# Kernel tuning notes

Hardware: AMD Instinct MI355X
Metric: run time of the kernel (lower is better)

Reference implementation:

```python
import jax, jax.numpy as jnp
import numpy as np

B, L, P = 65536, 512, 96
E_LIN, E = 14, 16
FFT = 512
TEMP = 0.07
K = 2
EPS = 1e-5


def setup_inputs() -> dict:
    key = jax.random.key(0)
    k0, k1, k2 = jax.random.split(key, 3)
    x = jax.random.normal(k0, (B, L), dtype=jnp.float32)
    Wg = jax.random.normal(k1, (E, FFT // 2), dtype=jnp.float32) * 0.02
    bg = jnp.zeros((E,), dtype=jnp.float32)
    Wr = jax.random.normal(k2, (E_LIN, P, L), dtype=jnp.float32) * 0.02
    br = jnp.zeros((E_LIN, P), dtype=jnp.float32)
    return {"x": x, "Wg": Wg, "bg": bg, "Wr": Wr, "br": br}


def _periodogram(x):
    # x: [B, L] -> normalized power spectrum [B, FFT//2]
    x0 = x - jnp.mean(x, axis=1, keepdims=True)
    dft = jnp.fft.fft(x0, n=FFT, axis=1) / np.float32(np.sqrt(FFT))
    dft = dft[:, : FFT // 2]
    I = dft.real ** 2 + dft.imag ** 2
    s = jnp.sum(I, axis=1, keepdims=True)
    s = jnp.where(s == 0, jnp.ones_like(s), s)
    return I / s


def reference(x, Wg, bg, Wr, br):
    # gating (eval mode: no noise, divide by temperature)
    I = _periodogram(x)                                  # [B, F/2]
    gate = (I @ Wg.T + bg) / TEMP                        # [B, E]
    topv, topi = jax.lax.top_k(gate, K)                  # [B, K]
    gates = jax.nn.softmax(topv, axis=1)                 # [B, K]

    # RLinear experts: RevIN(norm) -> Linear -> RevIN(denorm); stats detached
    mu = jax.lax.stop_gradient(jnp.mean(x, axis=1, keepdims=True))        # [B,1]
    sd = jax.lax.stop_gradient(jnp.sqrt(jnp.var(x, axis=1, keepdims=True) + EPS))
    xn = (x - mu) / sd                                   # [B, L]
    yr = jnp.einsum('bl,epl->bep', xn, Wr) + br          # [B, E_LIN, P]
    yr = yr * sd[:, :, None] + mu[:, :, None]

    mean_out = jnp.broadcast_to(jnp.mean(x, axis=1, keepdims=True), (x.shape[0], P))[:, None, :]
    naive_out = jnp.broadcast_to(x[:, -1:], (x.shape[0], P))[:, None, :]

    eo = jnp.concatenate([yr, mean_out, naive_out], axis=1)   # [B, E, P]
    sel = jnp.take_along_axis(eo, topi[:, :, None], axis=1)   # [B, K, P]
    out = jnp.sum(gates[:, :, None] * sel, axis=1)            # [B, P]
    return out
```

## Files before the change

### kernel.cpp

```cpp
#include <hip/hip_runtime.h>
#include <math.h>

#define NB_B 65536
#define NL   512
#define NP   96
#define NE   16
#define NEL  14
#define NF   256
#define TEMP_INV (1.0f/0.07f)
#define TAU  1e-5f
#define PI_D 3.14159265358979323846
#define MAXCHK 1280

typedef __attribute__((ext_vector_type(8))) short bf16x8;
typedef __attribute__((ext_vector_type(4))) float f32x4;


#define WS_PCNT     0
#define WS_PTK      16384
#define WS_PBASE    32768
#define WS_FLAGCNT  33792
#define WS_NCHK     33824
#define WS_FLAG     33856
#define WS_SSUM     296000
#define WS_WGT      301376
#define WS_BGT      317760
#define WS_TWF      317824
#define WS_TWD      319872
#define WS_REC      328064
#define WS_HDR      590208
#define WS_RIDX     1638784
#define WS_WRB      1900928
#define WS_DESC     3473792

__device__ __forceinline__ unsigned short f2bf(float f) {
    unsigned u = __float_as_uint(f);
    unsigned r = (u + 0x7fffu + ((u >> 16) & 1u)) >> 16;
    return (unsigned short)r;
}

__global__ __launch_bounds__(256) void k_prep(
    const float* __restrict__ Wg, const float* __restrict__ bg,
    const float* __restrict__ Wr,
    float* __restrict__ Ssum, float* __restrict__ WgE, float* __restrict__ bgT,
    float2* __restrict__ twf, double2* __restrict__ twd,
    int* __restrict__ pcnt, int* __restrict__ flagcnt,
    ushort4* __restrict__ Wrb)
{
    int g = blockIdx.x * 256 + threadIdx.x;
    {
        ushort4 o = make_ushort4(0, 0, 0, 0);
        if (g < NEL * NP * NL / 4) {
            float4 v = ((const float4*)Wr)[g];
            o.x = f2bf(v.x); o.y = f2bf(v.y); o.z = f2bf(v.z); o.w = f2bf(v.w);
        }
        Wrb[g] = o;
    }
    if (g < NEL * NP) {
        const float4* w = (const float4*)(Wr + (size_t)g * NL);
        float s = 0.f;
        for (int i = 0; i < NL / 4; i++) { float4 v = w[i]; s += v.x + v.y + v.z + v.w; }
        Ssum[g] = s;
    }
    if (g < 4096) {
        int c = g & 3, e = (g >> 2) & 15, f4 = g >> 6;
        WgE[g] = Wg[e * NF + f4 * 4 + c] * TEMP_INV;
    }
    if (g < NF) {
        double a = -2.0 * PI_D * (double)g / 512.0;
        twf[g] = make_float2((float)cos(a), (float)sin(a));
    }
    if (g < 512) {
        double a = -2.0 * PI_D * (double)g / 512.0;
        twd[g] = make_double2(cos(a), sin(a));
    }
    if (g < 256) pcnt[g << 4] = 0;
    if (g < NE) bgT[g] = bg[g] * TEMP_INV;
    if (g == 300) *flagcnt = 0;
}

__global__ __launch_bounds__(256) void k_gate(
    const float* __restrict__ x,
    const float4* __restrict__ WgE4, const float* __restrict__ bgT,
    const float2* __restrict__ twf,
    int* __restrict__ rec, float4* __restrict__ hdr,
    int* __restrict__ flaglist, int* __restrict__ flagcnt,
    int* __restrict__ pcnt)
{
    __shared__ float2 s_tw[256];
    __shared__ __align__(16) float2 s_z[4][576];
    float* s_Iv = (float*)&s_z[0][0];

    const int t = threadIdx.x;
    const int wv = t >> 6, l = t & 63;
    const int b0 = blockIdx.x * 8 + wv * 2;
    s_tw[t] = twf[t];

    const float* xa = x + (size_t)b0 * NL;
    const float* xb = xa + NL;
    float xr[8], xi[8];
#pragma unroll
    for (int k = 0; k < 8; k++) { xr[k] = xa[k * 64 + l]; xi[k] = xb[k * 64 + l]; }
    const float last_a = __shfl(xr[7], 63);
    const float last_b = __shfl(xi[7], 63);
    __syncthreads();

#pragma unroll
    for (int k = 0; k < 4; k++) {
        float2 w = s_tw[k * 64 + l];
        float ur = xr[k], ui = xi[k], vr = xr[k + 4], vi = xi[k + 4];
        xr[k] = ur + vr; xi[k] = ui + vi;
        float dr = ur - vr, di = ui - vi;
        xr[k + 4] = dr * w.x - di * w.y; xi[k + 4] = dr * w.y + di * w.x;
    }
    {
        const int kk[4] = {0, 1, 4, 5};
#pragma unroll
        for (int g2 = 0; g2 < 4; g2++) {
            int k = kk[g2];
            float2 w = s_tw[((k & 1) * 64 + l) << 1];
            float ur = xr[k], ui = xi[k], vr = xr[k + 2], vi = xi[k + 2];
            xr[k] = ur + vr; xi[k] = ui + vi;
            float dr = ur - vr, di = ui - vi;
            xr[k + 2] = dr * w.x - di * w.y; xi[k + 2] = dr * w.y + di * w.x;
        }
    }
    {
        float2 w = s_tw[l << 2];
#pragma unroll
        for (int k = 0; k < 8; k += 2) {
            float ur = xr[k], ui = xi[k], vr = xr[k + 1], vi = xi[k + 1];
            xr[k] = ur + vr; xi[k] = ui + vi;
            float dr = ur - vr, di = ui - vi;
            xr[k + 1] = dr * w.x - di * w.y; xi[k + 1] = dr * w.y + di * w.x;
        }
    }
#pragma unroll
    for (int st = 3; st < 9; st++) {
        const int half = 256 >> st;
        const int tt = (l & (half - 1)) << st;
        float2 w = s_tw[tt];
        const bool up = (l & half) != 0;
        const float sg = up ? -1.f : 1.f;
        const float cc = up ? w.x : 1.f;
        const float ss = up ? w.y : 0.f;
#pragma unroll
        for (int k = 0; k < 8; k++) {
            float pr = __shfl_xor(xr[k], half);
            float pi = __shfl_xor(xi[k], half);
            float tr = fmaf(sg, xr[k], pr);
            float ti = fmaf(sg, xi[k], pi);
            xr[k] = tr * cc - ti * ss;
            xi[k] = tr * ss + ti * cc;
        }
    }

#pragma unroll
    for (int k = 0; k < 8; k++) {
        int i = k * 64 + l;
        s_z[wv][i + (i >> 3)] = make_float2(xr[k], xi[k]);
    }

    float Ia[4], Ib[4];
    float psa = 0.f, psb = 0.f;
#pragma unroll
    for (int j = 0; j < 4; j++) {
        int f = (l << 2) | j;
        int i1_ = (int)(__brev((unsigned)f) >> 23);
        int i2_ = (int)(__brev((unsigned)((512 - f) & 511)) >> 23);
        float2 z1 = s_z[wv][i1_ + (i1_ >> 3)];
        float2 z2 = s_z[wv][i2_ + (i2_ >> 3)];
        float pr_ = z1.x + z2.x, qm = z1.y - z2.y;
        float qp = z1.y + z2.y, pm = z1.x - z2.x;
        float va = pr_ * pr_ + qm * qm;
        float vb = qp * qp + pm * pm;
        if (f == 0) { va = 0.f; vb = 0.f; }
        Ia[j] = va; Ib[j] = vb;
        psa += va; psb += vb;
    }
#pragma unroll
    for (int m = 1; m < 64; m <<= 1) {
        psa += __shfl_xor(psa, m); psb += __shfl_xor(psb, m);
    }
    const float psa_raw = psa, psb_raw = psb;
    if (psa == 0.f) psa = 1.f;
    if (psb == 0.f) psb = 1.f;
    const float inv_a = 1.f / psa, inv_b = 1.f / psb;

    const float2 Z0   = s_z[wv][0];
    const float2 Z256 = s_z[wv][1];

    float* wI = s_Iv + wv * 1152;
    const int io = (l << 2) + ((l >> 4) << 2);
    *(float4*)(wI + io)       = make_float4(Ia[0], Ia[1], Ia[2], Ia[3]);
    *(float4*)(wI + 272 + io) = make_float4(Ib[0], Ib[1], Ib[2], Ib[3]);

    const int e16 = l & 15, cq = l >> 4;
    const float bgv = bgT[e16];
    float accA = 0.f, accB = 0.f;
    const float* rA = wI + cq * 68;
    const float* rB = rA + 272;
#pragma unroll 4
    for (int jj = 0; jj < 16; jj++) {
        float4 ia = *(const float4*)(rA + 4 * jj);
        float4 ib = *(const float4*)(rB + 4 * jj);
        float4 w = WgE4[(cq * 16 + jj) * 16 + e16];
        accA += ia.x * w.x + ia.y * w.y + ia.z * w.z + ia.w * w.w;
        accB += ib.x * w.x + ib.y * w.y + ib.z * w.z + ib.w * w.w;
    }
    accA += __shfl_xor(accA, 16); accA += __shfl_xor(accA, 32);
    accB += __shfl_xor(accB, 16); accB += __shfl_xor(accB, 32);

    float v = ((l & 16) ? accB * inv_b : accA * inv_a) + bgv;

    float b0v = v; int b0i = e16;
#pragma unroll
    for (int m = 1; m < 16; m <<= 1) {
        float ov = __shfl_xor(b0v, m); int oi = __shfl_xor(b0i, m);
        if (ov > b0v || (ov == b0v && oi < b0i)) { b0v = ov; b0i = oi; }
    }
    float v1 = (e16 == b0i) ? -1e30f : v;
    float b1v = v1; int b1i = e16;
#pragma unroll
    for (int m = 1; m < 16; m <<= 1) {
        float ov = __shfl_xor(b1v, m); int oi = __shfl_xor(b1i, m);
        if (ov > b1v || (ov == b1v && oi < b1i)) { b1v = ov; b1i = oi; }
    }
    float v2 = (e16 == b1i) ? -1e30f : v1;
    float b2v = v2;
#pragma unroll
    for (int m = 1; m < 16; m <<= 1) {
        float ov = __shfl_xor(b2v, m);
        b2v = fmaxf(b2v, ov);
    }

    if (l == 0 || l == 16) {
        const int r = l >> 4;
        const int b = b0 + r;
        const float mu = (r ? Z0.y : Z0.x) * (1.f / 512.f);
        const float Jv = r ? Z256.y : Z256.x;
        const float ps = r ? psb_raw : psa_raw;
        const float sd = sqrtf((0.5f * ps + Jv * Jv) * (1.f / 262144.f) + 1e-5f);
        const float last = r ? last_b : last_a;
        const float w0 = 1.f / (1.f + expf(b1v - b0v));
        const int pid = b0i * 16 + b1i;
        rec[b] = pid;
        hdr[b] = make_float4(mu, sd, last, w0);
        atomicAdd(&pcnt[pid << 4], 1);
        if (b1v - b2v < TAU) {
            int pos = atomicAdd(flagcnt, 1);
            flaglist[pos] = b;
        }
    }
}

__global__ __launch_bounds__(256) void k_refine(
    const float* __restrict__ x, const double2* __restrict__ twd,
    const float* __restrict__ Wg, const float* __restrict__ bg,
    int* __restrict__ rec, float4* __restrict__ hdr,
    const int* __restrict__ flaglist, const int* __restrict__ flagcnt,
    int* __restrict__ pcnt)
{
    __shared__ double s_x[512];
    __shared__ double s_I[256];
    __shared__ double s_red[16];
    __shared__ double s_g[16];
    const int nf = *flagcnt;
    const int t = threadIdx.x;
    const int wid = t >> 6, lane = t & 63;
    for (int fi = blockIdx.x; fi < nf; fi += gridDim.x) {
        const int b = flaglist[fi];
        const float* xp = x + (size_t)b * NL;
        double v0 = (double)xp[t], v1 = (double)xp[t + 256];
        double lsum = v0 + v1;
        for (int m = 1; m < 64; m <<= 1) lsum += __shfl_xor(lsum, m);
        if (lane == 0) s_red[wid] = lsum;
        __syncthreads();
        double mu = (s_red[0] + s_red[1] + s_red[2] + s_red[3]) * (1.0 / 512.0);
        s_x[t] = v0 - mu; s_x[t + 256] = v1 - mu;
        __syncthreads();
        double2 w = twd[t];
        double pr = 1.0, pi = 0.0, cr = 0.0, ci = 0.0;
        for (int n = 0; n < 512; n++) {
            double xv = s_x[n];
            cr += xv * pr; ci += xv * pi;
            double t2 = pr * w.x - pi * w.y;
            pi = pr * w.y + pi * w.x;
            pr = t2;
        }
        double I = cr * cr + ci * ci;
        s_I[t] = I;
        double ls = I;
        for (int m = 1; m < 64; m <<= 1) ls += __shfl_xor(ls, m);
        if (lane == 0) s_red[8 + wid] = ls;
        __syncthreads();
        double stot = s_red[8] + s_red[9] + s_red[10] + s_red[11];
        if (stot == 0.0) stot = 1.0;
        if (t < 16) {
            double acc = 0.0;
            const float* wrow = Wg + t * NF;
            for (int f = 0; f < NF; f++) acc += s_I[f] * (double)wrow[f];
            s_g[t] = (acc / stot + (double)bg[t]) * (1.0 / 0.07);
        }
        __syncthreads();
        if (t == 0) {
            double c0 = -1e300, c1 = -1e300; int j0 = 0, j1 = 0;
            for (int i = 0; i < 16; i++) {
                double v = s_g[i];
                if (v > c0) { c1 = c0; j1 = j0; c0 = v; j0 = i; }
                else if (v > c1) { c1 = v; j1 = i; }
            }
            double e1 = exp(c1 - c0);
            float w0f = (float)(1.0 / (1.0 + e1));
            int newpid = j0 * 16 + j1;
            int old = rec[b];
            if (newpid != old) {
                atomicSub(&pcnt[old << 4], 1);
                atomicAdd(&pcnt[newpid << 4], 1);
                rec[b] = newpid;
            }
            ((float*)(hdr + b))[3] = w0f;
        }
        __syncthreads();
    }
}

__global__ __launch_bounds__(256) void k_scan(
    const int* __restrict__ pcnt, int* __restrict__ pbase, int* __restrict__ ptk,
    int* __restrict__ desc, int* __restrict__ nchk)
{
    __shared__ int s[256], c[256];
    const int t = threadIdx.x;
    const int n = pcnt[t << 4];
    s[t] = n;
    c[t] = (n + 63) >> 6;
    __syncthreads();
    for (int off = 1; off < 256; off <<= 1) {
        int v1 = (t >= off) ? s[t - off] : 0;
        int v2 = (t >= off) ? c[t - off] : 0;
        __syncthreads();
        s[t] += v1; c[t] += v2;
        __syncthreads();
    }
    int excl = t ? s[t - 1] : 0;
    int cexcl = t ? c[t - 1] : 0;
    pbase[t] = excl;
    ptk[t << 4] = excl;
    int myc = (n + 63) >> 6;
    for (int j = 0; j < myc; j++) desc[cexcl + j] = (t << 16) | j;
    if (t == 255) *nchk = cexcl + myc;
}

__global__ __launch_bounds__(256) void k_scatter(
    const int* __restrict__ rec, int* __restrict__ ptk, int* __restrict__ ridx)
{
    __shared__ int h[256], base_[256];
    const int t = threadIdx.x;
    const int b = blockIdx.x * 256 + t;
    h[t] = 0;
    __syncthreads();
    int pid = rec[b];
    int lo = atomicAdd(&h[pid], 1);
    __syncthreads();
    if (h[t]) base_[t] = atomicAdd(&ptk[t << 4], h[t]);
    __syncthreads();
    ridx[base_[pid] + lo] = b;
}

__global__ __launch_bounds__(256) void k_gemm(
    const float* __restrict__ x, const unsigned short* __restrict__ Wrb,
    const float* __restrict__ br, const float* __restrict__ Ssum,
    const float4* __restrict__ hdr, float* __restrict__ out,
    const int* __restrict__ pcnt, const int* __restrict__ pbase,
    const int* __restrict__ ridx,
    const int* __restrict__ desc, const int* __restrict__ nchk)
{
    __shared__ __align__(16) unsigned short sA[64 * 72];
    __shared__ __align__(16) unsigned short sB[2][96 * 72];
    __shared__ int    s_idx[64];
    __shared__ float4 s_hdr[64];
    __shared__ float  s_br[2][96], s_S[2][96];
    if ((int)blockIdx.x >= *nchk) return;
    const int d = desc[blockIdx.x];
    const int pid = d >> 16, cc = d & 0xffff;
    const int n = pcnt[pid << 4];
    const int base = pbase[pid];
    const int i0 = pid >> 4, i1 = pid & 15;
    const int t = threadIdx.x;
    const int lane = t & 63, wv = t >> 6;
    const int quad = lane >> 4, l16 = lane & 15;
    const int ar = t >> 2, asub = t & 3;
    if (t < 96) {
        s_br[0][t] = (i0 < NEL) ? br[i0 * NP + t] : 0.f;
        s_S [0][t] = (i0 < NEL) ? Ssum[i0 * NP + t] : 0.f;
        s_br[1][t] = (i1 < NEL) ? br[i1 * NP + t] : 0.f;
        s_S [1][t] = (i1 < NEL) ? Ssum[i1 * NP + t] : 0.f;
    }
    if (t < 64) {
        int g = cc * 64 + t;
        bool vld = g < n;
        int row = vld ? ridx[base + g] : -1;
        s_idx[t] = row;
        s_hdr[t] = vld ? hdr[row] : make_float4(0.f, 0.f, 0.f, 0.f);
    }
    const unsigned short* wb0 = Wrb + (size_t)i0 * NP * NL;
    const unsigned short* wb1 = Wrb + (size_t)i1 * NP * NL;
    __syncthreads();

    f32x4 acc[2][6];
#pragma unroll
    for (int ex = 0; ex < 2; ex++)
#pragma unroll
        for (int j = 0; j < 6; j++) acc[ex][j] = (f32x4){0.f, 0.f, 0.f, 0.f};
    int rr = s_idx[ar]; if (rr < 0) rr = s_idx[0];
    const float* xrow = x + (size_t)rr * NL + asub * 16;

    for (int kb = 0; kb < NL; kb += 64) {
        {
            const float4* src = (const float4*)(xrow + kb);
            unsigned short tmp[16];
#pragma unroll
            for (int i = 0; i < 4; i++) {
                float4 v = src[i];
                tmp[i * 4 + 0] = f2bf(v.x); tmp[i * 4 + 1] = f2bf(v.y);
                tmp[i * 4 + 2] = f2bf(v.z); tmp[i * 4 + 3] = f2bf(v.w);
            }
            unsigned short* dst = sA + ar * 72 + asub * 16;
            *(bf16x8*)dst       = *(bf16x8*)tmp;
            *(bf16x8*)(dst + 8) = *(bf16x8*)(tmp + 8);
        }
#pragma unroll
        for (int it = 0; it < 6; it++) {
            int ex = (it >= 3);
            int fl = t + (it - 3 * ex) * 256;
            int p = fl >> 3, kg = fl & 7;
            const unsigned short* wb = ex ? wb1 : wb0;
            bf16x8 v = *(const bf16x8*)(wb + (size_t)p * NL + kb + kg * 8);
            *(bf16x8*)(&sB[ex][p * 72 + kg * 8]) = v;
        }
        __syncthreads();
#pragma unroll
        for (int ks = 0; ks < 2; ks++) {
            bf16x8 af = *(const bf16x8*)(sA + (wv * 16 + l16) * 72 + ks * 32 + quad * 8);
#pragma unroll
            for (int ex = 0; ex < 2; ex++)
#pragma unroll
                for (int nt = 0; nt < 6; nt++) {
                    bf16x8 bf = *(const bf16x8*)(&sB[ex][(nt * 16 + l16) * 72 + ks * 32 + quad * 8]);
                    acc[ex][nt] = __builtin_amdgcn_mfma_f32_16x16x32_bf16(af, bf, acc[ex][nt], 0, 0, 0);
                }
        }
        __syncthreads();
    }
#pragma unroll
    for (int i = 0; i < 4; i++) {
        int rloc = wv * 16 + quad * 4 + i;
        int row = s_idx[rloc];
        if (row >= 0) {
            float4 h = s_hdr[rloc];
            float mu = h.x, sd = h.y, last = h.z, w0 = h.w, w1 = 1.f - w0;
            float* orow = out + (size_t)row * NP;
#pragma unroll
            for (int nt = 0; nt < 6; nt++) {
                int p = nt * 16 + l16;
                float v0 = (i0 < NEL) ? (mu + s_br[0][p] * sd - mu * s_S[0][p] + acc[0][nt][i])
                                      : (i0 == NEL ? mu : last);
                float v1 = (i1 < NEL) ? (mu + s_br[1][p] * sd - mu * s_S[1][p] + acc[1][nt][i])
                                      : (i1 == NEL ? mu : last);
                orow[p] = w0 * v0 + w1 * v1;
            }
        }
    }
}

extern "C" void kernel_launch(void* const* d_in, const int* in_sizes, int n_in,
                              void* d_out, int out_size, void* d_ws, size_t ws_size,
                              hipStream_t stream)
{
    const float* x  = (const float*)d_in[0];
    const float* Wg = (const float*)d_in[1];
    const float* bg = (const float*)d_in[2];
    const float* Wr = (const float*)d_in[3];
    const float* br = (const float*)d_in[4];
    float* out = (float*)d_out;
    char* ws = (char*)d_ws;

    int*     pcnt     = (int*)(ws + WS_PCNT);
    int*     ptk      = (int*)(ws + WS_PTK);
    int*     pbase    = (int*)(ws + WS_PBASE);
    int*     flagcnt  = (int*)(ws + WS_FLAGCNT);
    int*     nchk     = (int*)(ws + WS_NCHK);
    int*     flaglist = (int*)(ws + WS_FLAG);
    float*   Ssum     = (float*)(ws + WS_SSUM);
    float*   WgE      = (float*)(ws + WS_WGT);
    float*   bgT      = (float*)(ws + WS_BGT);
    float2*  twf      = (float2*)(ws + WS_TWF);
    double2* twd      = (double2*)(ws + WS_TWD);
    int*     rec      = (int*)(ws + WS_REC);
    float4*  hdr      = (float4*)(ws + WS_HDR);
    int*     ridx     = (int*)(ws + WS_RIDX);
    unsigned short* Wrb = (unsigned short*)(ws + WS_WRB);
    int*     desc     = (int*)(ws + WS_DESC);

    k_prep<<<dim3(768), dim3(256), 0, stream>>>(Wg, bg, Wr, Ssum, WgE, bgT, twf, twd,
                                                pcnt, flagcnt, (ushort4*)Wrb);
    k_gate<<<dim3(NB_B / 8), dim3(256), 0, stream>>>(x, (const float4*)WgE, bgT, twf,
                                                     rec, hdr, flaglist, flagcnt, pcnt);
    k_refine<<<dim3(512), dim3(256), 0, stream>>>(x, twd, Wg, bg, rec, hdr,
                                                  flaglist, flagcnt, pcnt);
    k_scan<<<dim3(1), dim3(256), 0, stream>>>(pcnt, pbase, ptk, desc, nchk);
    k_scatter<<<dim3(NB_B / 256), dim3(256), 0, stream>>>(rec, ptk, ridx);
    k_gemm<<<dim3(MAXCHK), dim3(256), 0, stream>>>(x, Wrb, br, Ssum, hdr, out,
                                                   pcnt, pbase, ridx, desc, nchk);
}
```

Measured before the change: 320.7 us.

## Cache bf16 copy of x in gate kernel and register-prefetch GEMM tiles

The gate kernel now writes a bf16 copy of x to workspace when space allows, so the GEMM reads half the bytes and skips the per-tile conversion. The GEMM prefetches the next A and B tiles into registers while the current tile is computed. FFT twiddles are held in registers instead of shared memory, and the last butterfly stage drops its trivial multiply. The cost is an extra bf16 write pass over x in the gate kernel, and the fast path depends on the workspace being large enough.

```diff
diff --git a/kernel.cpp b/kernel.cpp
--- a/kernel.cpp
+++ b/kernel.cpp
@@ -32,6 +32,7 @@
 #define WS_RIDX     1638784
 #define WS_WRB      1900928
 #define WS_DESC     3473792
+#define WS_XB16     3480064
 
 __device__ __forceinline__ unsigned short f2bf(float f) {
     unsigned u = __float_as_uint(f);
@@ -85,7 +86,7 @@
     const float2* __restrict__ twf,
     int* __restrict__ rec, float4* __restrict__ hdr,
     int* __restrict__ flaglist, int* __restrict__ flagcnt,
-    int* __restrict__ pcnt)
+    int* __restrict__ pcnt, unsigned short* __restrict__ xb16)
 {
     __shared__ float2 s_tw[256];
     __shared__ __align__(16) float2 s_z[4][576];
@@ -96,6 +97,14 @@
     const int b0 = blockIdx.x * 8 + wv * 2;
     s_tw[t] = twf[t];
 
+    const float2 w2 = twf[l << 2];
+    float2 wst[5];
+    wst[0] = twf[(l & 31) << 3];
+    wst[1] = twf[(l & 15) << 4];
+    wst[2] = twf[(l & 7) << 5];
+    wst[3] = twf[(l & 3) << 6];
+    wst[4] = twf[(l & 1) << 7];
+
     const float* xa = x + (size_t)b0 * NL;
     const float* xb = xa + NL;
     float xr[8], xi[8];
@@ -103,6 +112,16 @@
     for (int k = 0; k < 8; k++) { xr[k] = xa[k * 64 + l]; xi[k] = xb[k * 64 + l]; }
     const float last_a = __shfl(xr[7], 63);
     const float last_b = __shfl(xi[7], 63);
+
+    if (xb16) {
+        unsigned short* pa = xb16 + (size_t)b0 * NL + l;
+        unsigned short* pb = pa + NL;
+#pragma unroll
+        for (int k = 0; k < 8; k++) {
+            pa[k * 64] = f2bf(xr[k]);
+            pb[k * 64] = f2bf(xi[k]);
+        }
+    }
     __syncthreads();
 
 #pragma unroll
@@ -126,20 +145,18 @@
         }
     }
     {
-        float2 w = s_tw[l << 2];
 #pragma unroll
         for (int k = 0; k < 8; k += 2) {
             float ur = xr[k], ui = xi[k], vr = xr[k + 1], vi = xi[k + 1];
             xr[k] = ur + vr; xi[k] = ui + vi;
             float dr = ur - vr, di = ui - vi;
-            xr[k + 1] = dr * w.x - di * w.y; xi[k + 1] = dr * w.y + di * w.x;
-        }
-    }
-#pragma unroll
-    for (int st = 3; st < 9; st++) {
+            xr[k + 1] = dr * w2.x - di * w2.y; xi[k + 1] = dr * w2.y + di * w2.x;
+        }
+    }
+#pragma unroll
+    for (int st = 3; st < 8; st++) {
         const int half = 256 >> st;
-        const int tt = (l & (half - 1)) << st;
-        float2 w = s_tw[tt];
+        const float2 w = wst[st - 3];
         const bool up = (l & half) != 0;
         const float sg = up ? -1.f : 1.f;
         const float cc = up ? w.x : 1.f;
@@ -152,6 +169,16 @@
             float ti = fmaf(sg, xi[k], pi);
             xr[k] = tr * cc - ti * ss;
             xi[k] = tr * ss + ti * cc;
+        }
+    }
+    {
+        const float sg = (l & 1) ? -1.f : 1.f;
+#pragma unroll
+        for (int k = 0; k < 8; k++) {
+            float pr = __shfl_xor(xr[k], 1);
+            float pi = __shfl_xor(xi[k], 1);
+            xr[k] = fmaf(sg, xr[k], pr);
+            xi[k] = fmaf(sg, xi[k], pi);
         }
     }
 
@@ -367,8 +394,10 @@
     ridx[base_[pid] + lo] = b;
 }
 
+template<int XB>
 __global__ __launch_bounds__(256) void k_gemm(
-    const float* __restrict__ x, const unsigned short* __restrict__ Wrb,
+    const float* __restrict__ x, const unsigned short* __restrict__ xb16,
+    const unsigned short* __restrict__ Wrb,
     const float* __restrict__ br, const float* __restrict__ Ssum,
     const float4* __restrict__ hdr, float* __restrict__ out,
     const int* __restrict__ pcnt, const int* __restrict__ pbase,
@@ -403,8 +432,6 @@
         s_idx[t] = row;
         s_hdr[t] = vld ? hdr[row] : make_float4(0.f, 0.f, 0.f, 0.f);
     }
-    const unsigned short* wb0 = Wrb + (size_t)i0 * NP * NL;
-    const unsigned short* wb1 = Wrb + (size_t)i1 * NP * NL;
     __syncthreads();
 
     f32x4 acc[2][6];
@@ -412,33 +439,74 @@
     for (int ex = 0; ex < 2; ex++)
 #pragma unroll
         for (int j = 0; j < 6; j++) acc[ex][j] = (f32x4){0.f, 0.f, 0.f, 0.f};
+
     int rr = s_idx[ar]; if (rr < 0) rr = s_idx[0];
-    const float* xrow = x + (size_t)rr * NL + asub * 16;
+
+    unsigned boff[6];
+    unsigned short* bdst[6];
+    const unsigned short* wb[2];
+    wb[0] = Wrb + (size_t)i0 * NP * NL;
+    wb[1] = Wrb + (size_t)i1 * NP * NL;
+    int bex[6];
+#pragma unroll
+    for (int it = 0; it < 6; it++) {
+        int ex = (it >= 3);
+        int fl = t + (it - 3 * ex) * 256;
+        int p = fl >> 3, kg = fl & 7;
+        bex[it] = ex;
+        boff[it] = (unsigned)(p * NL + kg * 8);
+        bdst[it] = &sB[ex][p * 72 + kg * 8];
+    }
+    unsigned short* adst = sA + ar * 72 + asub * 16;
+
+    const unsigned short* xrow16 = xb16 + (size_t)rr * NL + asub * 16;
+    const float* xrowf = x + (size_t)rr * NL + asub * 16;
+
+    bf16x8 aR[2]; float4 fA[4]; bf16x8 bR[6];
+
+    if constexpr (XB) {
+        aR[0] = *(const bf16x8*)(xrow16);
+        aR[1] = *(const bf16x8*)(xrow16 + 8);
+    } else {
+#pragma unroll
+        for (int i = 0; i < 4; i++) fA[i] = ((const float4*)xrowf)[i];
+    }
+#pragma unroll
+    for (int it = 0; it < 6; it++) bR[it] = *(const bf16x8*)(wb[bex[it]] + boff[it]);
 
     for (int kb = 0; kb < NL; kb += 64) {
-        {
-            const float4* src = (const float4*)(xrow + kb);
+        if constexpr (XB) {
+            *(bf16x8*)adst       = aR[0];
+            *(bf16x8*)(adst + 8) = aR[1];
+        } else {
             unsigned short tmp[16];
 #pragma unroll
             for (int i = 0; i < 4; i++) {
-                float4 v = src[i];
+                float4 v = fA[i];
                 tmp[i * 4 + 0] = f2bf(v.x); tmp[i * 4 + 1] = f2bf(v.y);
                 tmp[i * 4 + 2] = f2bf(v.z); tmp[i * 4 + 3] = f2bf(v.w);
             }
-            unsigned short* dst = sA + ar * 72 + asub * 16;
-            *(bf16x8*)dst       = *(bf16x8*)tmp;
-            *(bf16x8*)(dst + 8) = *(bf16x8*)(tmp + 8);
-        }
-#pragma unroll
-        for (int it = 0; it < 6; it++) {
-            int ex = (it >= 3);
-            int fl = t + (it - 3 * ex) * 256;
-            int p = fl >> 3, kg = fl & 7;
-            const unsigned short* wb = ex ? wb1 : wb0;
-            bf16x8 v = *(const bf16x8*)(wb + (size_t)p * NL + kb + kg * 8);
-            *(bf16x8*)(&sB[ex][p * 72 + kg * 8]) = v;
-        }
-        __syncthreads();
+            *(bf16x8*)adst       = *(bf16x8*)tmp;
+            *(bf16x8*)(adst + 8) = *(bf16x8*)(tmp + 8);
+        }
+#pragma unroll
+        for (int it = 0; it < 6; it++) *(bf16x8*)bdst[it] = bR[it];
+        __syncthreads();
+
+        const int kn = kb + 64;
+        if (kn < NL) {
+            if constexpr (XB) {
+                aR[0] = *(const bf16x8*)(xrow16 + kn);
+                aR[1] = *(const bf16x8*)(xrow16 + kn + 8);
+            } else {
+#pragma unroll
+                for (int i = 0; i < 4; i++) fA[i] = ((const float4*)(xrowf + kn))[i];
+            }
+#pragma unroll
+            for (int it = 0; it < 6; it++)
+                bR[it] = *(const bf16x8*)(wb[bex[it]] + boff[it] + kn);
+        }
+
 #pragma unroll
         for (int ks = 0; ks < 2; ks++) {
             bf16x8 af = *(const bf16x8*)(sA + (wv * 16 + l16) * 72 + ks * 32 + quad * 8);
@@ -502,14 +570,22 @@
     unsigned short* Wrb = (unsigned short*)(ws + WS_WRB);
     int*     desc     = (int*)(ws + WS_DESC);
 
+    const size_t xb_bytes = (size_t)NB_B * NL * 2;
+    const int use_xb = (ws_size >= (size_t)WS_XB16 + xb_bytes);
+    unsigned short* xb16 = use_xb ? (unsigned short*)(ws + WS_XB16) : (unsigned short*)0;
+
     k_prep<<<dim3(768), dim3(256), 0, stream>>>(Wg, bg, Wr, Ssum, WgE, bgT, twf, twd,
                                                 pcnt, flagcnt, (ushort4*)Wrb);
     k_gate<<<dim3(NB_B / 8), dim3(256), 0, stream>>>(x, (const float4*)WgE, bgT, twf,
-                                                     rec, hdr, flaglist, flagcnt, pcnt);
+                                                     rec, hdr, flaglist, flagcnt, pcnt, xb16);
     k_refine<<<dim3(512), dim3(256), 0, stream>>>(x, twd, Wg, bg, rec, hdr,
                                                   flaglist, flagcnt, pcnt);
     k_scan<<<dim3(1), dim3(256), 0, stream>>>(pcnt, pbase, ptk, desc, nchk);
     k_scatter<<<dim3(NB_B / 256), dim3(256), 0, stream>>>(rec, ptk, ridx);
-    k_gemm<<<dim3(MAXCHK), dim3(256), 0, stream>>>(x, Wrb, br, Ssum, hdr, out,
-                                                   pcnt, pbase, ridx, desc, nchk);
-}
+    if (use_xb)
+        k_gemm<1><<<dim3(MAXCHK), dim3(256), 0, stream>>>(x, xb16, Wrb, br, Ssum, hdr, out,
+                                                          pcnt, pbase, ridx, desc, nchk);
+    else
+        k_gemm<0><<<dim3(MAXCHK), dim3(256), 0, stream>>>(x, xb16, Wrb, br, Ssum, hdr, out,
+                                                          pcnt, pbase, ridx, desc, nchk);
+}
```

Result: no change. 319.9 us (-0.3%).
